# Optimization experiments

Hardware: AMD Instinct MI355X
Metric: run time of the kernel (lower is better)

Reference implementation:

```python
import jax, jax.numpy as jnp
import numpy as np

N_T, N_Q = 32768, 4096
E_T, E_Q = 1048576, 131072
H = 128
VOCAB = 1001  # num_features + 1
NUM_LAYERS = 3


def _sage_conv(x, edge_index, Wl, bl, Wr):
    # PyG SAGEConv, aggr='mean': out = lin_l(mean_j x_j) + lin_r(x_i)
    src, dst = edge_index[0], edge_index[1]
    n = x.shape[0]
    agg = jax.ops.segment_sum(x[src], dst, num_segments=n)          # [n, H]
    cnt = jax.ops.segment_sum(jnp.ones((src.shape[0],), x.dtype), dst, num_segments=n)
    mean = agg / jnp.maximum(cnt, 1.0)[:, None]
    return mean @ Wl.T + bl + x @ Wr.T


def setup_inputs() -> dict:
    key = jax.random.key(0)
    ks = jax.random.split(key, 12)
    target_x = jax.random.randint(ks[0], (N_T,), 0, VOCAB, dtype=jnp.int64 if jax.config.jax_enable_x64 else jnp.int32)
    query_x = jax.random.randint(ks[1], (N_Q,), 0, VOCAB, dtype=target_x.dtype)
    target_edge_index = jax.random.randint(ks[2], (2, E_T), 0, N_T, dtype=target_x.dtype)
    query_edge_index = jax.random.randint(ks[3], (2, E_Q), 0, N_Q, dtype=target_x.dtype)
    mask = jax.random.bernoulli(ks[4], 0.5, (N_Q, N_T))
    emb = jax.random.normal(ks[5], (VOCAB, H), jnp.float32) * 0.02
    s = 1.0 / np.sqrt(H)
    Wl = jax.random.uniform(ks[6], (NUM_LAYERS, H, H), jnp.float32, -s, s)
    bl = jax.random.uniform(ks[7], (NUM_LAYERS, H), jnp.float32, -s, s)
    Wr = jax.random.uniform(ks[8], (NUM_LAYERS, H, H), jnp.float32, -s, s)
    return {"target_x": target_x, "query_x": query_x,
            "target_edge_index": target_edge_index, "query_edge_index": query_edge_index,
            "mask": mask, "emb": emb, "Wl": Wl, "bl": bl, "Wr": Wr}


def reference(target_x, query_x, target_edge_index, query_edge_index, mask, emb, Wl, bl, Wr):
    et = emb[target_x]  # [N_T, H]
    eq = emb[query_x]   # [N_Q, H]
    for i in range(NUM_LAYERS):
        et = jax.nn.elu(_sage_conv(et, target_edge_index, Wl[i], bl[i], Wr[i]))
        eq = jax.nn.elu(_sage_conv(eq, query_edge_index, Wl[i], bl[i], Wr[i]))
    fmask = mask.astype(jnp.float32)
    att = (eq @ et.T) * fmask / jnp.sqrt(jnp.float32(H)) + (-1e9) * (1.0 - fmask)
    att = jax.nn.softmax(att, axis=1)
    return att[None]  # [1, N_Q, N_T]
```

## Files before the change

### kernel.cpp

```cpp
#include <hip/hip_runtime.h>
#include <stdint.h>

#define N_T 32768
#define N_Q 4096
#define E_T 1048576
#define E_Q 131072
#define H   128
#define NL  3
#define VOCAB 1001

typedef float    f32x4 __attribute__((ext_vector_type(4)));
typedef int      i32x4 __attribute__((ext_vector_type(4)));
typedef _Float16 f16x8 __attribute__((ext_vector_type(8)));

__device__ __forceinline__ ushort f2h(float x){
  union{_Float16 h; ushort u;} c; c.h = (_Float16)x; return c.u;
}
__device__ __forceinline__ float h2f(unsigned u){
  union{ushort u; _Float16 h;} c; c.u = (ushort)u; return (float)c.h;
}

__global__ void init_k(int* cnt_t, int* cnt_q, float* rowsum, int* flag,
                       const unsigned* m,
                       const float* __restrict__ Wl, const float* __restrict__ Wr,
                       ushort* __restrict__ WH, ushort* __restrict__ WLo,
                       const float* __restrict__ emb, ushort* __restrict__ emb16){
  int b = blockIdx.x, t = threadIdx.x;
  if(b < 128){ cnt_t[b*256+t] = 0; }
  else if(b < 144){ cnt_q[(b-128)*256+t] = 0; }
  else if(b < 160){ rowsum[(b-144)*256+t] = 0.f; }
  else if(b == 160){
    if(t == 0) *flag = 0;
    __syncthreads();
    int f = 0;
    for(int j=t;j<4096;j+=256){
      unsigned v = m[j];
      if(v > 1u) f |= (v & 0xFEFEFEFEu) ? 2 : 1;
    }
    if(f) atomicOr(flag, f);
  }
  else if(b < 257){
    int i = (b-161)*256 + t;
    int k  = (i & 63) * 4;
    int c  = (i >> 6) & 127;
    int l  = i >> 13;
    const float* src = (k < 128)
        ? &Wl[((size_t)l*128 + c)*128 + k]
        : &Wr[((size_t)l*128 + c)*128 + (k-128)];
    float4 v = *(const float4*)src;
    ushort4 h, lo;
    h.x = f2h(v.x); lo.x = f2h(v.x - h2f(h.x));
    h.y = f2h(v.y); lo.y = f2h(v.y - h2f(h.y));
    h.z = f2h(v.z); lo.z = f2h(v.z - h2f(h.z));
    h.w = f2h(v.w); lo.w = f2h(v.w - h2f(h.w));
    size_t off = ((size_t)l*128 + c)*256 + k;
    *(ushort4*)&WH[off]  = h;
    *(ushort4*)&WLo[off] = lo;
  } else {
    int i = (b-257)*256 + t;
    if(i >= VOCAB*H/8) return;
    float4 v0 = ((const float4*)emb)[(size_t)i*2];
    float4 v1 = ((const float4*)emb)[(size_t)i*2 + 1];
    uint4 u;
    u.x = (unsigned)f2h(v0.x) | ((unsigned)f2h(v0.y)<<16);
    u.y = (unsigned)f2h(v0.z) | ((unsigned)f2h(v0.w)<<16);
    u.z = (unsigned)f2h(v1.x) | ((unsigned)f2h(v1.y)<<16);
    u.w = (unsigned)f2h(v1.z) | ((unsigned)f2h(v1.w)<<16);
    ((uint4*)emb16)[i] = u;
  }
}

__global__ void count2_k(const int* __restrict__ te, const int* __restrict__ qe,
                         int* cnt_t, int* cnt_q){
  int b = blockIdx.x;
  if(b < E_T/256){
    int i = b*256 + threadIdx.x;
    atomicAdd(&cnt_t[te[E_T + i]], 1);
  } else {
    int i = (b - E_T/256)*256 + threadIdx.x;
    atomicAdd(&cnt_q[qe[E_Q + i]], 1);
  }
}

__device__ __forceinline__ void scan_body(const int* cnt, int n, int* rp, int* pos){
  __shared__ int part[1024];
  int t = threadIdx.x;
  int chunk = (n + 1023) >> 10;
  int lo = t*chunk, hi = lo+chunk; if(hi>n) hi=n;
  int s = 0;
  int i = lo;
  for(; i+4 <= hi; i+=4){
    i32x4 v = *(const i32x4*)&cnt[i];
    s += v[0]+v[1]+v[2]+v[3];
  }
  for(; i < hi; i++) s += cnt[i];
  part[t] = s;
  __syncthreads();
  for(int off=1; off<1024; off<<=1){
    int v = (t >= off) ? part[t-off] : 0;
    __syncthreads();
    part[t] += v;
    __syncthreads();
  }
  int run = (t==0) ? 0 : part[t-1];
  i = lo;
  for(; i+4 <= hi; i+=4){
    i32x4 v = *(const i32x4*)&cnt[i];
    rp[i]=run;   pos[i]=run;   run += v[0];
    rp[i+1]=run; pos[i+1]=run; run += v[1];
    rp[i+2]=run; pos[i+2]=run; run += v[2];
    rp[i+3]=run; pos[i+3]=run; run += v[3];
  }
  for(; i < hi; i++){ rp[i]=run; pos[i]=run; run += cnt[i]; }
  if(t==0) rp[n] = part[1023];
}

__global__ void scan2_k(const int* cnt_t, int* rp_t, int* pos_t,
                        const int* cnt_q, int* rp_q, int* pos_q){
  if(blockIdx.x == 0) scan_body(cnt_t, N_T, rp_t, pos_t);
  else                scan_body(cnt_q, N_Q, rp_q, pos_q);
}

__global__ void fill2_k(const int* __restrict__ te, const int* __restrict__ qe,
                        int* pos_t, int* csr_t, int* pos_q, int* csr_q){
  int b = blockIdx.x;
  if(b < E_T/256){
    int i = b*256 + threadIdx.x;
    int p = atomicAdd(&pos_t[te[E_T + i]], 1);
    csr_t[p] = te[i];
  } else {
    int i = (b - E_T/256)*256 + threadIdx.x;
    int p = atomicAdd(&pos_q[qe[E_Q + i]], 1);
    csr_q[p] = qe[i];
  }
}

__device__ __forceinline__ void agg_body(const ushort* x, const int* nid,
    const ushort* emb16, const int* rp, const int* csr, ushort* agg,
    int wid, int lane){
  const unsigned* xw = (const unsigned*)x;
  const unsigned* ew = (const unsigned*)emb16;
  int rs = rp[wid], re = rp[wid+1];
  float px[8], py[8];
  #pragma unroll
  for(int q=0;q<8;q++){ px[q]=0.f; py[q]=0.f; }
  int j = rs;
  if(nid){
    for(; j+8 <= re; j+=8){
      #pragma unroll
      for(int q=0;q<8;q++){
        unsigned u = ew[(size_t)nid[csr[j+q]]*64 + lane];
        px[q] += h2f(u & 0xFFFFu); py[q] += h2f(u >> 16);
      }
    }
    for(; j < re; j++){
      unsigned u = ew[(size_t)nid[csr[j]]*64 + lane];
      px[0] += h2f(u & 0xFFFFu); py[0] += h2f(u >> 16);
    }
  } else {
    for(; j+8 <= re; j+=8){
      #pragma unroll
      for(int q=0;q<8;q++){
        unsigned u = xw[(size_t)csr[j+q]*64 + lane];
        px[q] += h2f(u & 0xFFFFu); py[q] += h2f(u >> 16);
      }
    }
    for(; j < re; j++){
      unsigned u = xw[(size_t)csr[j]*64 + lane];
      px[0] += h2f(u & 0xFFFFu); py[0] += h2f(u >> 16);
    }
  }
  float sx = ((px[0]+px[1]) + (px[2]+px[3])) + ((px[4]+px[5]) + (px[6]+px[7]));
  float sy = ((py[0]+py[1]) + (py[2]+py[3])) + ((py[4]+py[5]) + (py[6]+py[7]));
  int c = re - rs; if(c < 1) c = 1;
  float inv = 1.0f / (float)c;
  ((unsigned*)agg)[(size_t)wid*64 + lane] =
      (unsigned)f2h(sx*inv) | ((unsigned)f2h(sy*inv) << 16);
}

__global__ void agg2_k(const ushort* xt, const ushort* xq,
                       const int* nidt, const int* nidq, const ushort* emb16,
                       const int* rp_t, const int* csr_t,
                       const int* rp_q, const int* csr_q,
                       ushort* aggt, ushort* aggq){
  int b = blockIdx.x;
  int lane = threadIdx.x & 63;
  int wv = threadIdx.x >> 6;
  if(b < N_T/4){
    agg_body(xt, nidt, emb16, rp_t, csr_t, aggt, b*4 + wv, lane);
  } else {
    agg_body(xq, nidq, emb16, rp_q, csr_q, aggq, (b - N_T/4)*4 + wv, lane);
  }
}

__global__ __launch_bounds__(256,3) void layer2_k(
    const ushort* __restrict__ aggT, const ushort* __restrict__ xT,
    const int* __restrict__ nidT, ushort* __restrict__ outT,
    const ushort* __restrict__ aggQ, const ushort* __restrict__ xQ,
    const int* __restrict__ nidQ, ushort* __restrict__ outQ,
    const ushort* __restrict__ emb16,
    const ushort* __restrict__ WH, const ushort* __restrict__ WLo,
    const float* __restrict__ bl){
  __shared__ ushort SM3[3*128*64];
  ushort* SA = SM3;
  ushort* SH = SM3 + 8192;
  ushort* SL = SM3 + 16384;
  int bq = (int)blockIdx.x - (N_T/128);
  const ushort* agg   = (bq < 0) ? aggT : aggQ;
  const ushort* xprev = (bq < 0) ? xT   : xQ;
  const int*    nid   = (bq < 0) ? nidT : nidQ;
  ushort*       out16 = (bq < 0) ? outT : outQ;
  int r0g = ((bq < 0) ? (int)blockIdx.x : bq) * 128;
  int t = threadIdx.x;
  int lane = t & 63;
  int w = t >> 6;
  int wr = w >> 1, wc = w & 1;
  int fr = lane & 15, kg0 = lane >> 4;
  f32x4 acc[4][4] = {};
  for(int kt=0; kt<4; kt++){
    __syncthreads();
    int ko = (kt & 1) * 64;
    #pragma unroll
    for(int it=0; it<4; it++){
      int idx = t + it*256;
      int row = idx >> 3, k8 = idx & 7;
      int sw = (k8 ^ (row & 7)) * 8;
      uint4 av;
      if(kt < 2){
        av = *(const uint4*)&agg[(size_t)(r0g+row)*H + ko + k8*8];
      } else if(nid){
        av = *(const uint4*)&emb16[(size_t)nid[r0g+row]*H + ko + k8*8];
      } else {
        av = *(const uint4*)&xprev[(size_t)(r0g+row)*H + ko + k8*8];
      }
      *(uint4*)&SA[row*64 + sw] = av;
      *(uint4*)&SH[row*64 + sw] = *(const uint4*)&WH[row*256 + kt*64 + k8*8];
      *(uint4*)&SL[row*64 + sw] = *(const uint4*)&WLo[row*256 + kt*64 + k8*8];
    }
    __syncthreads();
    #pragma unroll
    for(int s=0; s<2; s++){
      int kg = s*4 + kg0;
      f16x8 a[4], bh[4], blo[4];
      #pragma unroll
      for(int m=0;m<4;m++){
        int ar = wr*64 + m*16 + fr;
        a[m] = *(const f16x8*)&SA[ar*64 + ((kg ^ (ar & 7)) << 3)];
      }
      #pragma unroll
      for(int n=0;n<4;n++){
        int bc = wc*64 + n*16 + fr;
        int ib = bc*64 + ((kg ^ (bc & 7)) << 3);
        bh[n]  = *(const f16x8*)&SH[ib];
        blo[n] = *(const f16x8*)&SL[ib];
      }
      #pragma unroll
      for(int m=0;m<4;m++)
        #pragma unroll
        for(int n=0;n<4;n++){
          acc[m][n] = __builtin_amdgcn_mfma_f32_16x16x32_f16(a[m], bh[n],  acc[m][n], 0,0,0);
          acc[m][n] = __builtin_amdgcn_mfma_f32_16x16x32_f16(a[m], blo[n], acc[m][n], 0,0,0);
        }
    }
  }
  __syncthreads();
  ushort* LT = SM3;
  #pragma unroll
  for(int n=0;n<4;n++){
    int c = wc*64 + n*16 + fr;
    float b = bl[c];
    #pragma unroll
    for(int m=0;m<4;m++){
      int r = wr*64 + m*16 + kg0*4;
      #pragma unroll
      for(int reg=0;reg<4;reg++){
        float v = acc[m][n][reg] + b;
        v = (v > 0.f) ? v : expm1f(v);
        LT[(r+reg)*128 + c] = f2h(v);
      }
    }
  }
  __syncthreads();
  #pragma unroll
  for(int i=0;i<8;i++){
    int idx = t + i*256;
    int row = idx >> 4, c8 = idx & 15;
    *(uint4*)&out16[(size_t)(r0g+row)*H + c8*8] = *(uint4*)&LT[row*128 + c8*8];
  }
}

__device__ __forceinline__ unsigned nib8(unsigned x, unsigned y){
  unsigned r = (x & 0xFu) | ((x>>4)&0xF0u) | ((x>>8)&0xF00u) | ((x>>12)&0xF000u);
  unsigned s = (y & 0xFu) | ((y>>4)&0xF0u) | ((y>>8)&0xF00u) | ((y>>12)&0xF000u);
  return r | (s<<16);
}
__device__ __forceinline__ unsigned pk4(unsigned u){
  return ((u & 0xFFu)       ? 1u : 0u) | ((u & 0xFF00u)     ? 2u : 0u)
       | ((u & 0xFF0000u)   ? 4u : 0u) | ((u & 0xFF000000u) ? 8u : 0u);
}

__device__ __forceinline__ void stage_mask_tile(const void* maskp, int mb,
    int gr0, int gc0, unsigned* MB, uint8_t* NB, unsigned* bitsOut, int t){
  if(mb & 2){
    const f32x4* base = (const f32x4*)maskp;
    #pragma unroll
    for(int i=0;i<16;i++){
      int idx = i*256 + t;
      int row = idx >> 5, c4 = idx & 31;
      f32x4 v = __builtin_nontemporal_load(
          &base[((size_t)(gr0+row)*N_T + gc0) / 4 + c4]);
      NB[row*32 + c4] = (uint8_t)((unsigned)(v[0]!=0.f) | ((unsigned)(v[1]!=0.f)<<1)
                                | ((unsigned)(v[2]!=0.f)<<2) | ((unsigned)(v[3]!=0.f)<<3));
    }
  } else if(mb & 1){
    const uint8_t* base = (const uint8_t*)maskp;
    #pragma unroll
    for(int i=0;i<16;i++){
      int idx = i*256 + t;
      int row = idx >> 5, c4 = idx & 31;
      unsigned u = __builtin_nontemporal_load(
          (const unsigned*)&base[(size_t)(gr0+row)*N_T + gc0 + c4*4]);
      NB[row*32 + c4] = (uint8_t)pk4(u);
    }
  } else {
    const i32x4* base = (const i32x4*)maskp;
    #pragma unroll
    for(int i=0;i<16;i++){
      int idx = i*256 + t;
      int row = idx >> 5, c4 = idx & 31;
      i32x4 v = __builtin_nontemporal_load(
          &base[((size_t)(gr0+row)*N_T + gc0) / 4 + c4]);
      NB[row*32 + c4] = (uint8_t)((unsigned)(v[0]!=0) | ((unsigned)(v[1]!=0)<<1)
                                | ((unsigned)(v[2]!=0)<<2) | ((unsigned)(v[3]!=0)<<3));
    }
  }
  __syncthreads();
  if(t < 128){
    uint4 a = *(const uint4*)&NB[t*32];
    uint4 b = *(const uint4*)&NB[t*32 + 16];
    unsigned w0 = nib8(a.x, a.y), w1 = nib8(a.z, a.w);
    unsigned w2 = nib8(b.x, b.y), w3 = nib8(b.z, b.w);
    MB[t*4]   = w0; MB[t*4+1] = w1;
    MB[t*4+2] = w2; MB[t*4+3] = w3;
    if(bitsOut){
      uint4 o; o.x=w0; o.y=w1; o.z=w2; o.w=w3;
      *(uint4*)&bitsOut[(size_t)(gr0 + t)*(N_T/32) + (gc0 >> 5)] = o;
    }
  }
}

__device__ __forceinline__ void att_tile(int bid, int& gc0, int& gr0){
  int xcd = bid & 7;
  int idx = bid >> 3;
  gc0 = (xcd*32 + (idx & 31)) * 128;
  gr0 = (idx >> 5) * 128;
}

__device__ __forceinline__ void qk_gemm(
    const ushort* __restrict__ A16, const ushort* __restrict__ B16,
    int abase, int bbase, int t, ushort* SM, f32x4 (&acc)[4][4]){
  ushort* AB = SM;
  ushort* BB = SM + 8192;
  int lane = t & 63;
  int w = t >> 6;
  int wr = w >> 1, wc = w & 1;
  int fr = lane & 15, kg0 = lane >> 4;
  for(int kt=0; kt<2; kt++){
    __syncthreads();
    #pragma unroll
    for(int it=0; it<4; it++){
      int idx = t + it*256;
      int row = idx >> 3, k8 = idx & 7;
      int sw = (k8 ^ (row & 7)) * 8;
      *(uint4*)&AB[row*64 + sw] = *(const uint4*)&A16[(size_t)(abase+row)*H + kt*64 + k8*8];
      *(uint4*)&BB[row*64 + sw] = *(const uint4*)&B16[(size_t)(bbase+row)*H + kt*64 + k8*8];
    }
    __syncthreads();
    #pragma unroll
    for(int s=0; s<2; s++){
      int kg = s*4 + kg0;
      f16x8 a[4], b[4];
      #pragma unroll
      for(int m=0;m<4;m++){
        int ar = wr*64 + m*16 + fr;
        a[m] = *(const f16x8*)&AB[ar*64 + ((kg ^ (ar & 7)) << 3)];
      }
      #pragma unroll
      for(int n=0;n<4;n++){
        int bc = wc*64 + n*16 + fr;
        b[n] = *(const f16x8*)&BB[bc*64 + ((kg ^ (bc & 7)) << 3)];
      }
      #pragma unroll
      for(int m=0;m<4;m++)
        #pragma unroll
        for(int n=0;n<4;n++)
          acc[m][n] = __builtin_amdgcn_mfma_f32_16x16x32_f16(a[m], b[n], acc[m][n], 0,0,0);
    }
  }
}

__global__ __launch_bounds__(256,4) void attsum_k(
    const ushort* __restrict__ eq16, const ushort* __restrict__ et16,
    const void* __restrict__ maskp, const int* __restrict__ flag,
    unsigned* __restrict__ bitsOut, float* __restrict__ rowsum){
  __shared__ ushort SM[2*128*64];
  __shared__ __align__(16) unsigned MB[512];
  __shared__ float RS[128][2];
  int t = threadIdx.x;
  int gc0, gr0;
  att_tile(blockIdx.x, gc0, gr0);
  int lane = t & 63;
  int w = t >> 6;
  int wr = w >> 1, wc = w & 1;
  int fr = lane & 15, kg0 = lane >> 4;

  int mb = *flag;
  stage_mask_tile(maskp, mb, gr0, gc0, MB, (uint8_t*)SM, bitsOut, t);

  f32x4 acc[4][4] = {};
  qk_gemm(et16, eq16, gc0, gr0, t, SM, acc);

  const float sc = 0.08838834764831845f;
  #pragma unroll
  for(int n=0;n<4;n++){
    int q = wc*64 + n*16 + fr;
    float s = 0.f;
    #pragma unroll
    for(int m=0;m<4;m++){
      unsigned wb = MB[q*4 + wr*2 + (m>>1)];
      int off = ((m&1)<<4) | (kg0<<2);
      s += ((wb>>(off+0))&1u) ? __expf(acc[m][n][0]*sc) : 0.f;
      s += ((wb>>(off+1))&1u) ? __expf(acc[m][n][1]*sc) : 0.f;
      s += ((wb>>(off+2))&1u) ? __expf(acc[m][n][2]*sc) : 0.f;
      s += ((wb>>(off+3))&1u) ? __expf(acc[m][n][3]*sc) : 0.f;
    }
    s += __shfl_xor(s, 16);
    s += __shfl_xor(s, 32);
    if(lane < 16) RS[q][wr] = s;
  }
  __syncthreads();
  if(t < 128) atomicAdd(&rowsum[gr0 + t], RS[t][0] + RS[t][1]);
}

__global__ __launch_bounds__(256,4) void attout_k(
    const ushort* __restrict__ eq16, const ushort* __restrict__ et16,
    const void* __restrict__ maskp, const int* __restrict__ flag,
    const unsigned* __restrict__ bitsIn, const float* __restrict__ rowsum,
    float* __restrict__ out){
  __shared__ ushort SM[2*128*64];
  __shared__ __align__(16) unsigned MB[512];
  __shared__ float IRS[128];
  int t = threadIdx.x;
  int gc0, gr0;
  att_tile(blockIdx.x, gc0, gr0);
  int lane = t & 63;
  int w = t >> 6;
  int wr = w >> 1, wc = w & 1;
  int fr = lane & 15, kg0 = lane >> 4;

  if(bitsIn){
    if(t < 128)
      *(uint4*)&MB[t*4] = *(const uint4*)&bitsIn[(size_t)(gr0 + t)*(N_T/32) + (gc0 >> 5)];
  } else {
    int mb = *flag;
    stage_mask_tile(maskp, mb, gr0, gc0, MB, (uint8_t*)SM, nullptr, t);
  }
  if(t < 128) IRS[t] = 1.0f / rowsum[gr0 + t];

  f32x4 acc[4][4] = {};
  qk_gemm(et16, eq16, gc0, gr0, t, SM, acc);

  const float sc = 0.08838834764831845f;
  #pragma unroll
  for(int n=0;n<4;n++){
    int q = wc*64 + n*16 + fr;
    float ir = IRS[q];
    size_t rb = (size_t)(gr0 + q)*N_T + gc0 + wr*64;
    #pragma unroll
    for(int m=0;m<4;m++){
      unsigned wb = MB[q*4 + wr*2 + (m>>1)];
      int off = ((m&1)<<4) | (kg0<<2);
      f32x4 o;
      o[0] = ((wb>>(off+0))&1u) ? __expf(acc[m][n][0]*sc)*ir : 0.f;
      o[1] = ((wb>>(off+1))&1u) ? __expf(acc[m][n][1]*sc)*ir : 0.f;
      o[2] = ((wb>>(off+2))&1u) ? __expf(acc[m][n][2]*sc)*ir : 0.f;
      o[3] = ((wb>>(off+3))&1u) ? __expf(acc[m][n][3]*sc)*ir : 0.f;
      __builtin_nontemporal_store(o, (f32x4*)&out[rb + m*16 + (kg0<<2)]);
    }
  }
}

extern "C" void kernel_launch(void* const* d_in, const int* in_sizes, int n_in,
                              void* d_out, int out_size, void* d_ws, size_t ws_size,
                              hipStream_t stream){
  const int* tx  = (const int*)d_in[0];
  const int* qx  = (const int*)d_in[1];
  const int* te  = (const int*)d_in[2];
  const int* qe  = (const int*)d_in[3];
  const void* mask = d_in[4];
  const float* emb = (const float*)d_in[5];
  const float* Wl  = (const float*)d_in[6];
  const float* bl  = (const float*)d_in[7];
  const float* Wr  = (const float*)d_in[8];
  float* out = (float*)d_out;

  ushort* et16 = (ushort*)d_ws;
  ushort* eq16 = et16 + (size_t)N_T*H;
  float* rowsum = (float*)((char*)d_ws + ((size_t)9 << 20));
  int*   flag   = (int*)(rowsum + N_Q);
  ushort* WH  = (ushort*)((char*)d_ws + ((size_t)10 << 20));
  ushort* WLo = WH + (size_t)NL*128*256;
  ushort* emb16 = (ushort*)((char*)d_ws + ((size_t)11 << 20));
  bool useBits = ws_size >= ((size_t)37 << 20);
  unsigned* bits = useBits ? (unsigned*)((char*)d_ws + ((size_t)19 << 20)) : nullptr;

  char* S = (char*)d_out;
  ushort* xt0  = (ushort*)(S);
  ushort* xt1  = (ushort*)(S + 8388608);
  ushort* aggt = (ushort*)(S + 16777216);
  ushort* xq0  = (ushort*)(S + 25165824);
  ushort* xq1  = (ushort*)(S + 26214400);
  ushort* aggq = (ushort*)(S + 27262976);
  int*   cnt_t = (int*)(S + 28311552);
  int*   rp_t  = cnt_t + N_T;
  int*   pos_t = rp_t + N_T + 1;
  int*   csr_t = pos_t + N_T;
  int*   cnt_q = csr_t + E_T;
  int*   rp_q  = cnt_q + N_Q;
  int*   pos_q = rp_q + N_Q + 1;
  int*   csr_q = pos_q + N_Q;

  init_k<<<320,256,0,stream>>>(cnt_t, cnt_q, rowsum, flag, (const unsigned*)mask,
                               Wl, Wr, WH, WLo, emb, emb16);
  count2_k<<<E_T/256 + E_Q/256,256,0,stream>>>(te, qe, cnt_t, cnt_q);
  scan2_k<<<2,1024,0,stream>>>(cnt_t, rp_t, pos_t, cnt_q, rp_q, pos_q);
  fill2_k<<<E_T/256 + E_Q/256,256,0,stream>>>(te, qe, pos_t, csr_t, pos_q, csr_q);

  ushort* outs_t[NL] = {xt0, xt1, et16};
  ushort* outs_q[NL] = {xq0, xq1, eq16};
  const ushort* cur_t = nullptr;
  const ushort* cur_q = nullptr;
  for(int l=0;l<NL;l++){
    const ushort* wh = WH  + (size_t)l*128*256;
    const ushort* wl = WLo + (size_t)l*128*256;
    const int* nidt = (l==0) ? tx : nullptr;
    const int* nidq = (l==0) ? qx : nullptr;
    agg2_k<<<N_T/4 + N_Q/4,256,0,stream>>>(cur_t, cur_q, nidt, nidq, emb16,
                                           rp_t, csr_t, rp_q, csr_q, aggt, aggq);
    layer2_k<<<N_T/128 + N_Q/128,256,0,stream>>>(aggt, cur_t, nidt, outs_t[l],
                                                 aggq, cur_q, nidq, outs_q[l],
                                                 emb16, wh, wl, bl+(size_t)l*H);
    cur_t = outs_t[l];
    cur_q = outs_q[l];
  }

  attsum_k<<<8192,256,0,stream>>>(eq16, et16, mask, flag, bits, rowsum);
  attout_k<<<8192,256,0,stream>>>(eq16, et16, mask, flag, bits, rowsum, out);
}
```

Measured before the change: 620.1 us.

## Spread mask bit-packing across earlier graph kernels as extra blocks

Mask-to-bitmask packing moves out of attsum_k and into extra blocks appended to the count, scan, fill, aggregation and layer kernels, 512 rows per launch. The aim is to overlap the mask read, which is bandwidth heavy, with the latency- and atomic-bound graph stages. attsum_k then reads precomputed bits instead of staging the raw mask tile. The risk is that the extra blocks slow the main blocks through shared bandwidth and occupancy, for example layer2_k's large shared-memory allocation, and that scan2_k launches 1024-thread blocks in which only 256 threads do packing.

After: 863.4 us. 39.2% more time.

```diff
diff --git a/kernel.cpp b/kernel.cpp
--- a/kernel.cpp
+++ b/kernel.cpp
@@ -18,6 +18,51 @@
 }
 __device__ __forceinline__ float h2f(unsigned u){
   union{ushort u; _Float16 h;} c; c.u = (ushort)u; return (float)c.h;
+}
+__device__ __forceinline__ unsigned pk4(unsigned u){
+  return ((u & 0xFFu)       ? 1u : 0u) | ((u & 0xFF00u)     ? 2u : 0u)
+       | ((u & 0xFF0000u)   ? 4u : 0u) | ((u & 0xFF000000u) ? 8u : 0u);
+}
+
+__device__ __forceinline__ void pack_row(const void* maskp, int mb,
+                                         unsigned* bits, int row, int t){
+  size_t rbase = (size_t)row * N_T;
+  if(mb & 2){
+    const f32x4* mp = (const f32x4*)((const float*)maskp + rbase);
+    for(int c = t; c < 1024; c += 256){
+      unsigned w = 0;
+      #pragma unroll
+      for(int i=0;i<8;i++){
+        f32x4 v = __builtin_nontemporal_load(&mp[c*8 + i]);
+        w |= ((unsigned)(v[0]!=0.f) | ((unsigned)(v[1]!=0.f)<<1)
+            | ((unsigned)(v[2]!=0.f)<<2) | ((unsigned)(v[3]!=0.f)<<3)) << (i*4);
+      }
+      bits[(size_t)row*1024 + c] = w;
+    }
+  } else if(mb & 1){
+    const uint8_t* mp = (const uint8_t*)maskp + rbase;
+    for(int c = t; c < 1024; c += 256){
+      unsigned w = 0;
+      #pragma unroll
+      for(int i=0;i<8;i++){
+        unsigned u = *(const unsigned*)&mp[c*32 + i*4];
+        w |= pk4(u) << (i*4);
+      }
+      bits[(size_t)row*1024 + c] = w;
+    }
+  } else {
+    const i32x4* mp = (const i32x4*)((const int*)maskp + rbase);
+    for(int c = t; c < 1024; c += 256){
+      unsigned w = 0;
+      #pragma unroll
+      for(int i=0;i<8;i++){
+        i32x4 v = __builtin_nontemporal_load(&mp[c*8 + i]);
+        w |= ((unsigned)(v[0]!=0) | ((unsigned)(v[1]!=0)<<1)
+            | ((unsigned)(v[2]!=0)<<2) | ((unsigned)(v[3]!=0)<<3)) << (i*4);
+      }
+      bits[(size_t)row*1024 + c] = w;
+    }
+  }
 }
 
 __global__ void init_k(int* cnt_t, int* cnt_q, float* rowsum, int* flag,
@@ -70,9 +115,16 @@
   }
 }
 
+#define CNT_MAIN (E_T/256 + E_Q/256)
 __global__ void count2_k(const int* __restrict__ te, const int* __restrict__ qe,
-                         int* cnt_t, int* cnt_q){
+                         int* cnt_t, int* cnt_q,
+                         const void* maskp, const int* flag,
+                         unsigned* bits, int packBase){
   int b = blockIdx.x;
+  if(b >= CNT_MAIN){
+    if(bits) pack_row(maskp, *flag, bits, packBase + b - CNT_MAIN, threadIdx.x);
+    return;
+  }
   if(b < E_T/256){
     int i = b*256 + threadIdx.x;
     atomicAdd(&cnt_t[te[E_T + i]], 1);
@@ -116,14 +168,28 @@
 }
 
 __global__ void scan2_k(const int* cnt_t, int* rp_t, int* pos_t,
-                        const int* cnt_q, int* rp_q, int* pos_q){
-  if(blockIdx.x == 0) scan_body(cnt_t, N_T, rp_t, pos_t);
-  else                scan_body(cnt_q, N_Q, rp_q, pos_q);
+                        const int* cnt_q, int* rp_q, int* pos_q,
+                        const void* maskp, const int* flag,
+                        unsigned* bits, int packBase){
+  int b = blockIdx.x;
+  if(b >= 2){
+    if(bits && threadIdx.x < 256)
+      pack_row(maskp, *flag, bits, packBase + b - 2, threadIdx.x);
+    return;
+  }
+  if(b == 0) scan_body(cnt_t, N_T, rp_t, pos_t);
+  else       scan_body(cnt_q, N_Q, rp_q, pos_q);
 }
 
 __global__ void fill2_k(const int* __restrict__ te, const int* __restrict__ qe,
-                        int* pos_t, int* csr_t, int* pos_q, int* csr_q){
+                        int* pos_t, int* csr_t, int* pos_q, int* csr_q,
+                        const void* maskp, const int* flag,
+                        unsigned* bits, int packBase){
   int b = blockIdx.x;
+  if(b >= CNT_MAIN){
+    if(bits) pack_row(maskp, *flag, bits, packBase + b - CNT_MAIN, threadIdx.x);
+    return;
+  }
   if(b < E_T/256){
     int i = b*256 + threadIdx.x;
     int p = atomicAdd(&pos_t[te[E_T + i]], 1);
@@ -178,12 +244,19 @@
       (unsigned)f2h(sx*inv) | ((unsigned)f2h(sy*inv) << 16);
 }
 
+#define AGG_MAIN (N_T/4 + N_Q/4)
 __global__ void agg2_k(const ushort* xt, const ushort* xq,
                        const int* nidt, const int* nidq, const ushort* emb16,
                        const int* rp_t, const int* csr_t,
                        const int* rp_q, const int* csr_q,
-                       ushort* aggt, ushort* aggq){
+                       ushort* aggt, ushort* aggq,
+                       const void* maskp, const int* flag,
+                       unsigned* bits, int packBase){
   int b = blockIdx.x;
+  if(b >= AGG_MAIN){
+    if(bits) pack_row(maskp, *flag, bits, packBase + b - AGG_MAIN, threadIdx.x);
+    return;
+  }
   int lane = threadIdx.x & 63;
   int wv = threadIdx.x >> 6;
   if(b < N_T/4){
@@ -193,6 +266,7 @@
   }
 }
 
+#define LAY_MAIN (N_T/128 + N_Q/128)
 __global__ __launch_bounds__(256,3) void layer2_k(
     const ushort* __restrict__ aggT, const ushort* __restrict__ xT,
     const int* __restrict__ nidT, ushort* __restrict__ outT,
@@ -200,8 +274,14 @@
     const int* __restrict__ nidQ, ushort* __restrict__ outQ,
     const ushort* __restrict__ emb16,
     const ushort* __restrict__ WH, const ushort* __restrict__ WLo,
-    const float* __restrict__ bl){
+    const float* __restrict__ bl,
+    const void* maskp, const int* flag,
+    unsigned* bits, int packBase){
   __shared__ ushort SM3[3*128*64];
+  if((int)blockIdx.x >= LAY_MAIN){
+    if(bits) pack_row(maskp, *flag, bits, packBase + (int)blockIdx.x - LAY_MAIN, threadIdx.x);
+    return;
+  }
   ushort* SA = SM3;
   ushort* SH = SM3 + 8192;
   ushort* SL = SM3 + 16384;
@@ -294,13 +374,9 @@
   unsigned s = (y & 0xFu) | ((y>>4)&0xF0u) | ((y>>8)&0xF00u) | ((y>>12)&0xF000u);
   return r | (s<<16);
 }
-__device__ __forceinline__ unsigned pk4(unsigned u){
-  return ((u & 0xFFu)       ? 1u : 0u) | ((u & 0xFF00u)     ? 2u : 0u)
-       | ((u & 0xFF0000u)   ? 4u : 0u) | ((u & 0xFF000000u) ? 8u : 0u);
-}
 
 __device__ __forceinline__ void stage_mask_tile(const void* maskp, int mb,
-    int gr0, int gc0, unsigned* MB, uint8_t* NB, unsigned* bitsOut, int t){
+    int gr0, int gc0, unsigned* MB, uint8_t* NB, int t){
   if(mb & 2){
     const f32x4* base = (const f32x4*)maskp;
     #pragma unroll
@@ -338,14 +414,10 @@
   if(t < 128){
     uint4 a = *(const uint4*)&NB[t*32];
     uint4 b = *(const uint4*)&NB[t*32 + 16];
-    unsigned w0 = nib8(a.x, a.y), w1 = nib8(a.z, a.w);
-    unsigned w2 = nib8(b.x, b.y), w3 = nib8(b.z, b.w);
-    MB[t*4]   = w0; MB[t*4+1] = w1;
-    MB[t*4+2] = w2; MB[t*4+3] = w3;
-    if(bitsOut){
-      uint4 o; o.x=w0; o.y=w1; o.z=w2; o.w=w3;
-      *(uint4*)&bitsOut[(size_t)(gr0 + t)*(N_T/32) + (gc0 >> 5)] = o;
-    }
+    MB[t*4]   = nib8(a.x, a.y);
+    MB[t*4+1] = nib8(a.z, a.w);
+    MB[t*4+2] = nib8(b.x, b.y);
+    MB[t*4+3] = nib8(b.z, b.w);
   }
 }
 
@@ -402,7 +474,7 @@
 __global__ __launch_bounds__(256,4) void attsum_k(
     const ushort* __restrict__ eq16, const ushort* __restrict__ et16,
     const void* __restrict__ maskp, const int* __restrict__ flag,
-    unsigned* __restrict__ bitsOut, float* __restrict__ rowsum){
+    const unsigned* __restrict__ bitsIn, float* __restrict__ rowsum){
   __shared__ ushort SM[2*128*64];
   __shared__ __align__(16) unsigned MB[512];
   __shared__ float RS[128][2];
@@ -414,8 +486,13 @@
   int wr = w >> 1, wc = w & 1;
   int fr = lane & 15, kg0 = lane >> 4;
 
-  int mb = *flag;
-  stage_mask_tile(maskp, mb, gr0, gc0, MB, (uint8_t*)SM, bitsOut, t);
+  if(bitsIn){
+    if(t < 128)
+      *(uint4*)&MB[t*4] = *(const uint4*)&bitsIn[(size_t)(gr0 + t)*(N_T/32) + (gc0 >> 5)];
+  } else {
+    int mb = *flag;
+    stage_mask_tile(maskp, mb, gr0, gc0, MB, (uint8_t*)SM, t);
+  }
 
   f32x4 acc[4][4] = {};
   qk_gemm(et16, eq16, gc0, gr0, t, SM, acc);
@@ -463,7 +540,7 @@
       *(uint4*)&MB[t*4] = *(const uint4*)&bitsIn[(size_t)(gr0 + t)*(N_T/32) + (gc0 >> 5)];
   } else {
     int mb = *flag;
-    stage_mask_tile(maskp, mb, gr0, gc0, MB, (uint8_t*)SM, nullptr, t);
+    stage_mask_tile(maskp, mb, gr0, gc0, MB, (uint8_t*)SM, t);
   }
   if(t < 128) IRS[t] = 1.0f / rowsum[gr0 + t];
 
@@ -513,6 +590,7 @@
   ushort* emb16 = (ushort*)((char*)d_ws + ((size_t)11 << 20));
   bool useBits = ws_size >= ((size_t)37 << 20);
   unsigned* bits = useBits ? (unsigned*)((char*)d_ws + ((size_t)19 << 20)) : nullptr;
+  int nPack = useBits ? 512 : 0;
 
   char* S = (char*)d_out;
   ushort* xt0  = (ushort*)(S);
@@ -532,24 +610,33 @@
 
   init_k<<<320,256,0,stream>>>(cnt_t, cnt_q, rowsum, flag, (const unsigned*)mask,
                                Wl, Wr, WH, WLo, emb, emb16);
-  count2_k<<<E_T/256 + E_Q/256,256,0,stream>>>(te, qe, cnt_t, cnt_q);
-  scan2_k<<<2,1024,0,stream>>>(cnt_t, rp_t, pos_t, cnt_q, rp_q, pos_q);
-  fill2_k<<<E_T/256 + E_Q/256,256,0,stream>>>(te, qe, pos_t, csr_t, pos_q, csr_q);
+  count2_k<<<CNT_MAIN + nPack,256,0,stream>>>(te, qe, cnt_t, cnt_q,
+                                              mask, flag, bits, 0);
+  scan2_k<<<2 + nPack,1024,0,stream>>>(cnt_t, rp_t, pos_t, cnt_q, rp_q, pos_q,
+                                       mask, flag, bits, 512);
+  fill2_k<<<CNT_MAIN + nPack,256,0,stream>>>(te, qe, pos_t, csr_t, pos_q, csr_q,
+                                             mask, flag, bits, 1024);
 
   ushort* outs_t[NL] = {xt0, xt1, et16};
   ushort* outs_q[NL] = {xq0, xq1, eq16};
   const ushort* cur_t = nullptr;
   const ushort* cur_q = nullptr;
+  int aggBase[NL] = {1536, 2560, 3584};
+  int layBase[NL] = {2048, 3072, 0};
   for(int l=0;l<NL;l++){
     const ushort* wh = WH  + (size_t)l*128*256;
     const ushort* wl = WLo + (size_t)l*128*256;
     const int* nidt = (l==0) ? tx : nullptr;
     const int* nidq = (l==0) ? qx : nullptr;
-    agg2_k<<<N_T/4 + N_Q/4,256,0,stream>>>(cur_t, cur_q, nidt, nidq, emb16,
-                                           rp_t, csr_t, rp_q, csr_q, aggt, aggq);
-    layer2_k<<<N_T/128 + N_Q/128,256,0,stream>>>(aggt, cur_t, nidt, outs_t[l],
-                                                 aggq, cur_q, nidq, outs_q[l],
-                                                 emb16, wh, wl, bl+(size_t)l*H);
+    int aN = nPack;
+    int lN = (l < 2) ? nPack : 0;
+    agg2_k<<<AGG_MAIN + aN,256,0,stream>>>(cur_t, cur_q, nidt, nidq, emb16,
+                                           rp_t, csr_t, rp_q, csr_q, aggt, aggq,
+                                           mask, flag, bits, aggBase[l]);
+    layer2_k<<<LAY_MAIN + lN,256,0,stream>>>(aggt, cur_t, nidt, outs_t[l],
+                                             aggq, cur_q, nidq, outs_q[l],
+                                             emb16, wh, wl, bl+(size_t)l*H,
+                                             mask, flag, bits, layBase[l]);
     cur_t = outs_t[l];
     cur_q = outs_q[l];
   }
```
